# Optimization experiments

Hardware: AMD Instinct MI355X
Metric: run time of the kernel (lower is better)

Reference implementation:

```python
import jax, jax.numpy as jnp
import numpy as np

INF = 10000.0

# ---------- differentiable (jax) pieces ----------

def _embed(x, W1, b1, W2, b2):
    # nn.Sequential(Linear, Dropout(eval=identity), ReLU, Linear, ReLU)
    h = jax.nn.relu(x @ W1.T + b1)
    return jax.nn.relu(h @ W2.T + b2)


def _cdist(a, b):
    # batched euclidean cdist with zero-safe sqrt (matches torch.cdist values)
    sq = (jnp.sum(a * a, -1)[:, :, None]
          + jnp.sum(b * b, -1)[:, None, :]
          - 2.0 * jnp.einsum('bnd,bmd->bnm', a, b))
    sq = jnp.maximum(sq, 0.0)
    safe = jnp.where(sq > 0, sq, 1.0)
    return jnp.where(sq > 0, jnp.sqrt(safe), 0.0)


def _edit_costs(x_s, x_t, W1, b1, W2, b2, virtual, B, N):
    D = W2.shape[0]
    es = _embed(x_s, W1, b1, W2, b2).reshape(B, N, D)
    et = _embed(x_t, W1, b1, W2, b2).reshape(B, N, D)
    v = _embed(virtual[None, :], W1, b1, W2, b2)          # [1, D]
    vb = jnp.broadcast_to(v[None, :, :], (B, 1, D))
    es = jnp.concatenate([es, vb], axis=1)                # [B, N+1, D]
    et = jnp.concatenate([et, vb], axis=1)
    d = _cdist(es, et)                                    # [B, N+1, N+1]
    # per-pair normalization: d / sum(d) * (len_s * len_t)
    d = d / jnp.sum(d, axis=(1, 2), keepdims=True) * float(N * N)
    return d

# ---------- host-side LSAPE (replaces scipy.optimize.linear_sum_assignment) ----------

def _lsap(C):
    # Jonker-Volgenant / shortest augmenting path, square cost matrix.
    n = C.shape[0]
    u = np.zeros(n + 1)
    v = np.zeros(n + 1)
    p = np.zeros(n + 1, np.int64)    # p[j] = row matched to column j (1-indexed)
    way = np.zeros(n + 1, np.int64)
    for i in range(1, n + 1):
        p[0] = i
        j0 = 0
        minv = np.full(n + 1, np.inf)
        used = np.zeros(n + 1, bool)
        while True:
            used[j0] = True
            i0 = p[j0]
            free = np.nonzero(~used)[0]
            cur = C[i0 - 1, free - 1] - u[i0] - v[free]
            better = cur < minv[free]
            minv[free] = np.where(better, cur, minv[free])
            way[free] = np.where(better, j0, way[free])
            k = int(np.argmin(minv[free]))
            j1 = int(free[k])
            delta = minv[free][k]
            u[p[used]] += delta
            v[used] -= delta
            minv[free] -= delta
            j0 = j1
            if p[j0] == 0:
                break
        while j0 != 0:
            j1 = int(way[j0])
            p[j0] = p[j1]
            j0 = j1
    rows = p[1:] - 1
    cols = np.arange(n)
    return rows, cols


def _lsape(ec, n, m):
    # ec: (n+1, m+1) edit costs with virtual row/col; build (n+m)x(n+m) LSAPE matrix
    C = np.zeros((n + m, n + m))
    C[:n, :m] = ec[:n, :m]
    C[n:, :m] = INF
    C[:n, m:] = INF
    C[np.arange(n, n + m), np.arange(m)] = ec[n, :m]       # insertions
    C[np.arange(n), np.arange(m, m + n)] = ec[:n, m]       # deletions
    C[~np.isfinite(C)] = INF
    q, p = _lsap(C)
    A = np.zeros((n + 1, m + 1), np.int64)
    A[np.minimum(q, n), np.minimum(p, m)] = 1
    A[-1, -1] = 0
    return A

# ---------- harness ----------

def setup_inputs() -> dict:
    B, N, FIN, D = 16, 128, 512, 512
    key = jax.random.key(0)
    ks = jax.random.split(key, 7)
    s1 = 1.0 / np.sqrt(FIN)
    s2 = 1.0 / np.sqrt(D)
    return {
        'x_s': jax.random.normal(ks[0], (B * N, FIN), jnp.float32),
        'x_t': jax.random.normal(ks[1], (B * N, FIN), jnp.float32),
        'W1': jax.random.uniform(ks[2], (D, FIN), jnp.float32, -s1, s1),
        'b1': jax.random.uniform(ks[3], (D,), jnp.float32, -s1, s1),
        'W2': jax.random.uniform(ks[4], (D, D), jnp.float32, -s2, s2),
        'b2': jax.random.uniform(ks[5], (D,), jnp.float32, -s2, s2),
        'virtual': jax.random.uniform(ks[6], (FIN,), jnp.float32),
        'npairs': 16,
        'n_nodes': 128,
    }


def reference(x_s, x_t, W1, b1, W2, b2, virtual, npairs, n_nodes):
    B, N = int(npairs), int(n_nodes)
    edit = _edit_costs(x_s, x_t, W1, b1, W2, b2, virtual, B, N)  # [B, N+1, N+1]
    ec_np = np.asarray(jax.device_get(edit), np.float64)
    aligns = np.stack([_lsape(ec_np[i], N, N) for i in range(B)])
    A = jnp.asarray(aligns)                                      # [B, N+1, N+1] int
    geds = jnp.sum(A * edit, axis=(1, 2)) / float(2 * N)         # / (len_s + len_t)
    return (A, edit, geds)
```

## Files before the change

kernel.cpp:

```cpp
#include <hip/hip_runtime.h>

#define BATCH 16
#define NNODE 128
#define DIM 512
#define NP1 129
#define EDSZ (NP1 * NP1)
#define BIGF 3.0e38f

__global__ __launch_bounds__(256) void gemm2_nt_relu(
    const float* __restrict__ X0, const float* __restrict__ X1,
    const float* __restrict__ W, const float* __restrict__ bias,
    float* __restrict__ Y0, float* __restrict__ Y1,
    int M, int N, int K) {
  const float* X = blockIdx.z ? X1 : X0;
  float* Y = blockIdx.z ? Y1 : Y0;
  __shared__ float sA[32][68];
  __shared__ float sB[32][68];
  const int tid = threadIdx.x;
  const int m0 = blockIdx.x * 64;
  const int n0 = blockIdx.y * 64;
  const int tm = tid / 16, tn = tid % 16;
  const int lr = tid >> 2;
  const int lk8 = (tid & 3) * 8;
  float acc[4][4] = {};
  for (int k0 = 0; k0 < K; k0 += 32) {
    const float* xa = X + (size_t)(m0 + lr) * K + k0 + lk8;
    const float* wb = W + (size_t)(n0 + lr) * K + k0 + lk8;
    float4 a0 = *(const float4*)(xa);
    float4 a1 = *(const float4*)(xa + 4);
    float4 b0 = *(const float4*)(wb);
    float4 b1 = *(const float4*)(wb + 4);
    sA[lk8 + 0][lr] = a0.x; sA[lk8 + 1][lr] = a0.y;
    sA[lk8 + 2][lr] = a0.z; sA[lk8 + 3][lr] = a0.w;
    sA[lk8 + 4][lr] = a1.x; sA[lk8 + 5][lr] = a1.y;
    sA[lk8 + 6][lr] = a1.z; sA[lk8 + 7][lr] = a1.w;
    sB[lk8 + 0][lr] = b0.x; sB[lk8 + 1][lr] = b0.y;
    sB[lk8 + 2][lr] = b0.z; sB[lk8 + 3][lr] = b0.w;
    sB[lk8 + 4][lr] = b1.x; sB[lk8 + 5][lr] = b1.y;
    sB[lk8 + 6][lr] = b1.z; sB[lk8 + 7][lr] = b1.w;
    __syncthreads();
#pragma unroll
    for (int k = 0; k < 32; ++k) {
      const float4 a = *(const float4*)&sA[k][tm * 4];
      const float4 b = *(const float4*)&sB[k][tn * 4];
      acc[0][0] = fmaf(a.x, b.x, acc[0][0]);
      acc[0][1] = fmaf(a.x, b.y, acc[0][1]);
      acc[0][2] = fmaf(a.x, b.z, acc[0][2]);
      acc[0][3] = fmaf(a.x, b.w, acc[0][3]);
      acc[1][0] = fmaf(a.y, b.x, acc[1][0]);
      acc[1][1] = fmaf(a.y, b.y, acc[1][1]);
      acc[1][2] = fmaf(a.y, b.z, acc[1][2]);
      acc[1][3] = fmaf(a.y, b.w, acc[1][3]);
      acc[2][0] = fmaf(a.z, b.x, acc[2][0]);
      acc[2][1] = fmaf(a.z, b.y, acc[2][1]);
      acc[2][2] = fmaf(a.z, b.z, acc[2][2]);
      acc[2][3] = fmaf(a.z, b.w, acc[2][3]);
      acc[3][0] = fmaf(a.w, b.x, acc[3][0]);
      acc[3][1] = fmaf(a.w, b.y, acc[3][1]);
      acc[3][2] = fmaf(a.w, b.z, acc[3][2]);
      acc[3][3] = fmaf(a.w, b.w, acc[3][3]);
    }
    __syncthreads();
  }
#pragma unroll
  for (int i = 0; i < 4; ++i) {
    int m = m0 + tm * 4 + i;
#pragma unroll
    for (int j = 0; j < 4; ++j) {
      int n = n0 + tn * 4 + j;
      Y[(size_t)m * N + n] = fmaxf(acc[i][j] + bias[n], 0.f);
    }
  }
}

__global__ __launch_bounds__(256) void virt_embed(
    const float* __restrict__ x,
    const float* __restrict__ W1, const float* __restrict__ b1,
    const float* __restrict__ W2, const float* __restrict__ b2,
    float* __restrict__ e_v) {
  __shared__ float sx[DIM];
  __shared__ float sh[DIM];
  for (int k = threadIdx.x; k < DIM; k += 256) sx[k] = x[k];
  __syncthreads();
  for (int n = threadIdx.x; n < DIM; n += 256) {
    const float* w = W1 + (size_t)n * DIM;
    float s = 0.f;
    for (int k = 0; k < DIM; k += 4) {
      float4 wv = *(const float4*)(w + k);
      s = fmaf(sx[k + 0], wv.x, s);
      s = fmaf(sx[k + 1], wv.y, s);
      s = fmaf(sx[k + 2], wv.z, s);
      s = fmaf(sx[k + 3], wv.w, s);
    }
    sh[n] = fmaxf(s + b1[n], 0.f);
  }
  __syncthreads();
  for (int n = threadIdx.x; n < DIM; n += 256) {
    const float* w = W2 + (size_t)n * DIM;
    float s = 0.f;
    for (int k = 0; k < DIM; k += 4) {
      float4 wv = *(const float4*)(w + k);
      s = fmaf(sh[k + 0], wv.x, s);
      s = fmaf(sh[k + 1], wv.y, s);
      s = fmaf(sh[k + 2], wv.z, s);
      s = fmaf(sh[k + 3], wv.w, s);
    }
    e_v[n] = fmaxf(s + b2[n], 0.f);
  }
}

__global__ __launch_bounds__(256) void cdist_kernel(
    const float* __restrict__ es, const float* __restrict__ et,
    const float* __restrict__ ev, float* __restrict__ d) {
  const int b = blockIdx.z;
  const int i0 = blockIdx.x * 32;
  const int j0 = blockIdx.y * 32;
  __shared__ float sA[32][33];
  __shared__ float sB[32][33];
  const int tid = threadIdx.x;
  const int ty = tid / 16, tx = tid % 16;
  const int lr = tid / 8;
  const int lk4 = (tid % 8) * 4;
  const int gi = i0 + lr;
  const int gj = j0 + lr;
  const float* pa = (gi < NNODE) ? (es + ((size_t)b * NNODE + gi) * DIM) : ev;
  const float* pb = (gj < NNODE) ? (et + ((size_t)b * NNODE + gj) * DIM) : ev;
  float acc[2][2] = {};
  for (int k0 = 0; k0 < DIM; k0 += 32) {
    float4 av = *(const float4*)(pa + k0 + lk4);
    float4 bv = *(const float4*)(pb + k0 + lk4);
    sA[lr][lk4 + 0] = av.x; sA[lr][lk4 + 1] = av.y;
    sA[lr][lk4 + 2] = av.z; sA[lr][lk4 + 3] = av.w;
    sB[lr][lk4 + 0] = bv.x; sB[lr][lk4 + 1] = bv.y;
    sB[lr][lk4 + 2] = bv.z; sB[lr][lk4 + 3] = bv.w;
    __syncthreads();
#pragma unroll 8
    for (int k = 0; k < 32; ++k) {
      float a0 = sA[ty * 2 + 0][k], a1 = sA[ty * 2 + 1][k];
      float b0 = sB[tx * 2 + 0][k], b1 = sB[tx * 2 + 1][k];
      float d00 = a0 - b0, d01 = a0 - b1, d10 = a1 - b0, d11 = a1 - b1;
      acc[0][0] = fmaf(d00, d00, acc[0][0]);
      acc[0][1] = fmaf(d01, d01, acc[0][1]);
      acc[1][0] = fmaf(d10, d10, acc[1][0]);
      acc[1][1] = fmaf(d11, d11, acc[1][1]);
    }
    __syncthreads();
  }
#pragma unroll
  for (int i = 0; i < 2; ++i) {
    int gi2 = i0 + ty * 2 + i;
#pragma unroll
    for (int j = 0; j < 2; ++j) {
      int gj2 = j0 + tx * 2 + j;
      if (gi2 < NP1 && gj2 < NP1)
        d[(size_t)b * EDSZ + gi2 * NP1 + gj2] = sqrtf(acc[i][j]);
    }
  }
}

__global__ __launch_bounds__(256) void batch_sum(
    const float* __restrict__ d, float* __restrict__ sums) {
  const int b = blockIdx.x;
  double s = 0.0;
  for (int idx = threadIdx.x; idx < EDSZ; idx += 256)
    s += (double)d[(size_t)b * EDSZ + idx];
  __shared__ double red[256];
  red[threadIdx.x] = s;
  __syncthreads();
  for (int off = 128; off; off >>= 1) {
    if (threadIdx.x < off) red[threadIdx.x] += red[threadIdx.x + off];
    __syncthreads();
  }
  if (threadIdx.x == 0) sums[b] = (float)red[0];
}

__global__ __launch_bounds__(256) void normalize_kernel(
    const float* __restrict__ d, const float* __restrict__ sums,
    float* __restrict__ edit) {
  int idx = blockIdx.x * 256 + threadIdx.x;
  if (idx < BATCH * EDSZ) {
    int b = idx / EDSZ;
    edit[idx] = d[idx] / sums[b] * (float)(NNODE * NNODE);
  }
}

__device__ __forceinline__ unsigned key_of(float m, int col) {
  return (__float_as_uint(m) & 0xFFFFFF80u) | (unsigned)col;
}

template <int CTRL>
__device__ __forceinline__ unsigned dpp_umin_step(unsigned x) {
  const unsigned o = (unsigned)__builtin_amdgcn_update_dpp(
      (int)0xFFFFFFFFu, (int)x, CTRL, 0xf, 0xf, false);
  return o < x ? o : x;
}

__device__ __forceinline__ unsigned wave_umin_key(unsigned x) {
  x = dpp_umin_step<0x111>(x);
  x = dpp_umin_step<0x112>(x);
  x = dpp_umin_step<0x114>(x);
  x = dpp_umin_step<0x118>(x);
  x = dpp_umin_step<0x142>(x);
  x = dpp_umin_step<0x143>(x);
  return (unsigned)__builtin_amdgcn_readlane((int)x, 63);
}

template <int CTRL>
__device__ __forceinline__ void dpp_umin2_step(unsigned& m1, unsigned& m2) {
  const unsigned o1 = (unsigned)__builtin_amdgcn_update_dpp(
      (int)0xFFFFFFFFu, (int)m1, CTRL, 0xf, 0xf, false);
  const unsigned o2 = (unsigned)__builtin_amdgcn_update_dpp(
      (int)0xFFFFFFFFu, (int)m2, CTRL, 0xf, 0xf, false);
  const unsigned lo = m1 < o1 ? m1 : o1;
  const unsigned hi = m1 < o1 ? o1 : m1;
  const unsigned yo = m2 < o2 ? m2 : o2;
  m1 = lo;
  m2 = hi < yo ? hi : yo;
}

__device__ __forceinline__ void wave_umin2_key(unsigned a, unsigned b,
                                               unsigned& k1, unsigned& k2) {
  unsigned m1 = a < b ? a : b;
  unsigned m2 = a < b ? b : a;
  dpp_umin2_step<0x111>(m1, m2);
  dpp_umin2_step<0x112>(m1, m2);
  dpp_umin2_step<0x114>(m1, m2);
  dpp_umin2_step<0x118>(m1, m2);
  dpp_umin2_step<0x142>(m1, m2);
  dpp_umin2_step<0x143>(m1, m2);
  k1 = (unsigned)__builtin_amdgcn_readlane((int)m1, 63);
  k2 = (unsigned)__builtin_amdgcn_readlane((int)m2, 63);
}

__device__ __forceinline__ float fsel2(float a0, float a1, int s) {
  return (s == 0) ? a0 : a1;
}
__device__ __forceinline__ int isel2(int a0, int a1, int s) {
  return (s == 0) ? a0 : a1;
}
__device__ __forceinline__ float readlane_f32(float x, int lane) {
  return __uint_as_float(
      (unsigned)__builtin_amdgcn_readlane((int)__float_as_uint(x), lane));
}

__global__ __launch_bounds__(64) void lsap_kernel(
    const float* __restrict__ edit, float* __restrict__ Aout,
    float* __restrict__ geds) {
  const int b = blockIdx.x;
  const float* ec = edit + (size_t)b * EDSZ;
  float* A = Aout + (size_t)b * EDSZ;
  const int lane = threadIdx.x;
  const int cbase = lane * 2;

  __shared__ float D[NNODE * NNODE];

  for (int idx = lane; idx < NNODE * NNODE; idx += 64) {
    const int i = idx >> 7, j = idx & 127;
    const float sub = ec[i * NP1 + j];
    const float di = ec[i * NP1 + NNODE] + ec[NNODE * NP1 + j];
    D[idx] = fminf(sub, di);
  }
  for (int idx = lane; idx < EDSZ; idx += 64) A[idx] = 0.f;
  __syncthreads();

  float u0 = 0.f, u1 = 0.f;
  float v0 = 0.f, v1 = 0.f;
  float m0, m1;
  int w0 = 0, w1 = 0;
  int p0 = 0, p1 = 0;
  int x0 = 0, x1 = 0;

  int y0 = 0, y1 = 0;
  {
    float c0 = BIGF, c1 = BIGF;
    for (int r = 0; r < NNODE; ++r) {
      const float2 f = *(const float2*)&D[r * NNODE + cbase];
      if (f.x < c0) { c0 = f.x; y0 = r; }
      if (f.y < c1) { c1 = f.y; y1 = r; }
    }
    v0 = c0; v1 = c1;
  }

  unsigned long long ra0 = 0, ra1 = 0;
  for (int j = 0; j < NNODE; ++j) {
    const int jl = j >> 1, jq = j & 1;
    const int i1 = __builtin_amdgcn_readlane(isel2(y0, y1, jq), jl);
    const int bit = i1 & 63;
    const unsigned long long msk = (i1 < 64) ? ra0 : ra1;
    if (!((msk >> bit) & 1ull)) {
      if (i1 < 64) ra0 |= 1ull << bit; else ra1 |= 1ull << bit;
      if (lane == jl) {
        if (jq == 0) p0 = i1 + 1;
        else p1 = i1 + 1;
      }
      if (lane == (i1 >> 1)) {
        if ((i1 & 1) == 0) x0 = j + 1;
        else x1 = j + 1;
      }
    }
  }

  for (int ii = 0; ii < NNODE; ++ii) {
    const int xj = __builtin_amdgcn_readlane(isel2(x0, x1, ii & 1), ii >> 1);
    if (xj == 0) continue;
    const int j1 = xj - 1;
    const float2 f = *(const float2*)&D[ii * NNODE + cbase];
    float r0 = fmaxf(f.x - v0, 0.f);
    float r1 = fmaxf(f.y - v1, 0.f);
    if (cbase + 0 == j1) r0 = BIGF;
    if (cbase + 1 == j1) r1 = BIGF;
    const unsigned ka = key_of(r0, cbase + 0);
    const unsigned kb = key_of(r1, cbase + 1);
    const unsigned kmin = wave_umin_key(ka < kb ? ka : kb);
    const int jm = (int)(kmin & 127u);
    const float umin = readlane_f32(fsel2(r0, r1, jm & 1), jm >> 1);
    if (lane == (j1 >> 1)) {
      if ((j1 & 1) == 0) v0 -= umin; else v1 -= umin;
    }
    if (lane == (ii >> 1)) {
      if ((ii & 1) == 0) u0 = umin; else u1 = umin;
    }
  }

  {
    const int nfree0 =
        NNODE - __builtin_popcountll(ra0) - __builtin_popcountll(ra1);
    const int budget = 2 * nfree0 + 8;
    for (int step = 0; step < budget; ++step) {
      const unsigned long long fm0 = ~ra0, fm1 = ~ra1;
      int i;
      if (fm0) i = __builtin_ctzll(fm0);
      else if (fm1) i = 64 + __builtin_ctzll(fm1);
      else break;

      const float2 f = *(const float2*)&D[i * NNODE + cbase];
      const float r0 = fmaxf(f.x - v0, 0.f);
      const float r1 = fmaxf(f.y - v1, 0.f);
      unsigned k1, k2;
      wave_umin2_key(key_of(r0, cbase + 0), key_of(r1, cbase + 1), k1, k2);
      const int j1 = (int)(k1 & 127u), j2 = (int)(k2 & 127u);
      const float u1v = readlane_f32(fsel2(r0, r1, j1 & 1), j1 >> 1);
      const float u2v = readlane_f32(fsel2(r0, r1, j2 & 1), j2 >> 1);

      int jt = j1;
      int i1 = __builtin_amdgcn_readlane(isel2(p0, p1, j1 & 1), j1 >> 1);
      if (u1v < u2v) {
        const float dv = u2v - u1v;
        if (lane == (j1 >> 1)) {
          if ((j1 & 1) == 0) v0 -= dv; else v1 -= dv;
        }
      } else if (i1 != 0) {
        jt = j2;
        i1 = __builtin_amdgcn_readlane(isel2(p0, p1, j2 & 1), j2 >> 1);
      }
      if (lane == (jt >> 1)) {
        if ((jt & 1) == 0) p0 = i + 1; else p1 = i + 1;
      }
      if (lane == (i >> 1)) {
        if ((i & 1) == 0) u0 = u2v; else u1 = u2v;
      }
      if (i < 64) ra0 |= 1ull << i; else ra1 |= 1ull << (i - 64);
      if (i1 != 0) {
        const int rr = i1 - 1;
        if (rr < 64) ra0 &= ~(1ull << rr); else ra1 &= ~(1ull << (rr - 64));
        if (lane == (rr >> 1)) {
          if ((rr & 1) == 0) u0 = 0.f; else u1 = 0.f;
        }
      }
    }
  }

  for (int ii = 0; ii < NNODE; ++ii) {
    const unsigned long long amsk = (ii < 64) ? ra0 : ra1;
    if ((amsk >> (ii & 63)) & 1ull) continue;
    const int i = ii + 1;

    unsigned cused = 0, rused = 0;
    m0 = m1 = BIGF;
    int j0 = 0;
    int i0 = i;
    for (int guard = 0; guard <= NNODE; ++guard) {
      if (j0 > 0 && lane == ((j0 - 1) >> 1)) {
        if (((j0 - 1) & 1) == 0) { cused |= 1u; m0 = BIGF; }
        else { cused |= 2u; m1 = BIGF; }
      }
      if (lane == ((i0 - 1) >> 1)) rused |= 1u << ((i0 - 1) & 1);

      const float u_i0 = readlane_f32(fsel2(u0, u1, (i0 - 1) & 1), (i0 - 1) >> 1);

      const float2 f = *(const float2*)&D[(i0 - 1) * NNODE + cbase];

      const bool f0 = !(cused & 1u), f1 = !(cused & 2u);
      {
        float cur = fmaxf(f.x - u_i0 - v0, 0.f);
        bool up = f0 && (cur < m0);
        m0 = up ? cur : m0; w0 = up ? j0 : w0;
      }
      {
        float cur = fmaxf(f.y - u_i0 - v1, 0.f);
        bool up = f1 && (cur < m1);
        m1 = up ? cur : m1; w1 = up ? j0 : w1;
      }

      const unsigned ka = key_of(m0, cbase + 0);
      const unsigned kb = key_of(m1, cbase + 1);
      const unsigned kmin = wave_umin_key(ka < kb ? ka : kb);
      const int jcol = (int)(kmin & 127u);
      const float delta = readlane_f32(fsel2(m0, m1, jcol & 1), jcol >> 1);
      const int j1 = jcol + 1;

      if (!f0) v0 -= delta; else m0 = fmaxf(m0 - delta, 0.f);
      if (!f1) v1 -= delta; else m1 = fmaxf(m1 - delta, 0.f);
      if (rused & 1u) u0 += delta;
      if (rused & 2u) u1 += delta;

      const int pj1 = __builtin_amdgcn_readlane(
          isel2(p0, p1, (j1 - 1) & 1), (j1 - 1) >> 1);
      j0 = j1;
      if (pj1 == 0) break;
      i0 = pj1;
    }

    int jc = j0;
    while (jc != 0) {
      const int cl = (jc - 1) >> 1, cq = (jc - 1) & 1;
      const int jp = __builtin_amdgcn_readlane(isel2(w0, w1, cq), cl);
      const int js = (jp == 0) ? 1 : jp;
      const int pvr = __builtin_amdgcn_readlane(
          isel2(p0, p1, (js - 1) & 1), (js - 1) >> 1);
      const int pv = (jp == 0) ? i : pvr;
      if (lane == cl) {
        if (cq == 0) p0 = pv;
        else p1 = pv;
      }
      jc = jp;
    }
  }

  double contrib = 0.0;
  {
    const int pr[2] = {p0, p1};
#pragma unroll
    for (int q = 0; q < 2; ++q) {
      const int j = cbase + q;
      const int i = pr[q] - 1;
      const float sub = ec[i * NP1 + j];
      const float di = ec[i * NP1 + NNODE] + ec[NNODE * NP1 + j];
      if (sub < di) {
        A[i * NP1 + j] = 1.f;
        contrib += (double)sub;
      } else {
        A[i * NP1 + NNODE] = 1.f;
        A[NNODE * NP1 + j] = 1.f;
        contrib += (double)di;
      }
    }
  }
#pragma unroll
  for (int off = 32; off; off >>= 1) contrib += __shfl_xor(contrib, off);
  if (lane == 0) geds[b] = (float)(contrib / 256.0);
}

extern "C" void kernel_launch(void* const* d_in, const int* in_sizes, int n_in,
                              void* d_out, int out_size, void* d_ws, size_t ws_size,
                              hipStream_t stream) {
  const float* x_s  = (const float*)d_in[0];
  const float* x_t  = (const float*)d_in[1];
  const float* W1   = (const float*)d_in[2];
  const float* b1   = (const float*)d_in[3];
  const float* W2   = (const float*)d_in[4];
  const float* b2   = (const float*)d_in[5];
  const float* virt = (const float*)d_in[6];

  const int M = BATCH * NNODE;

  float* ws    = (float*)d_ws;
  float* h_s   = ws;
  float* h_t   = h_s + (size_t)M * DIM;
  float* e_s   = h_t + (size_t)M * DIM;
  float* e_t   = e_s + (size_t)M * DIM;
  float* e_v   = e_t + (size_t)M * DIM;
  float* d_raw = e_v + DIM;
  float* sums  = d_raw + (size_t)BATCH * EDSZ;

  float* Aout = (float*)d_out;
  float* edit = Aout + (size_t)BATCH * EDSZ;
  float* geds = edit + (size_t)BATCH * EDSZ;

  dim3 gblk(M / 64, DIM / 64, 2);
  virt_embed<<<1, 256, 0, stream>>>(virt, W1, b1, W2, b2, e_v);
  gemm2_nt_relu<<<gblk, 256, 0, stream>>>(x_s, x_t, W1, b1, h_s, h_t, M, DIM, DIM);
  gemm2_nt_relu<<<gblk, 256, 0, stream>>>(h_s, h_t, W2, b2, e_s, e_t, M, DIM, DIM);

  cdist_kernel<<<dim3(5, 5, BATCH), 256, 0, stream>>>(e_s, e_t, e_v, d_raw);
  batch_sum<<<BATCH, 256, 0, stream>>>(d_raw, sums);
  normalize_kernel<<<(BATCH * EDSZ + 255) / 256, 256, 0, stream>>>(d_raw, sums, edit);
  lsap_kernel<<<BATCH, 64, 0, stream>>>(edit, Aout, geds);
}
```

Before: 823.6 us.

## Interleave two LSAP problems per wavefront and precompute reduced cost matrix

```diff
diff --git a/kernel.cpp b/kernel.cpp
--- a/kernel.cpp
+++ b/kernel.cpp
@@ -184,6 +184,18 @@
   }
 }
 
+__global__ __launch_bounds__(256) void build_D(
+    const float* __restrict__ edit, float* __restrict__ Dg) {
+  int idx = blockIdx.x * 256 + threadIdx.x;
+  if (idx < BATCH * NNODE * NNODE) {
+    const int b = idx >> 14;
+    const int rc = idx & 16383;
+    const int i = rc >> 7, j = rc & 127;
+    const float* ec = edit + (size_t)b * EDSZ;
+    Dg[idx] = fminf(ec[i * NP1 + j], ec[i * NP1 + NNODE] + ec[NNODE * NP1 + j]);
+  }
+}
+
 __device__ __forceinline__ unsigned key_of(float m, int col) {
   return (__float_as_uint(m) & 0xFFFFFF80u) | (unsigned)col;
 }
@@ -243,203 +255,267 @@
       (unsigned)__builtin_amdgcn_readlane((int)__float_as_uint(x), lane));
 }
 
-__global__ __launch_bounds__(64) void lsap_kernel(
-    const float* __restrict__ edit, float* __restrict__ Aout,
-    float* __restrict__ geds) {
-  const int b = blockIdx.x;
-  const float* ec = edit + (size_t)b * EDSZ;
-  float* A = Aout + (size_t)b * EDSZ;
+__global__ __launch_bounds__(64) void lsap2_kernel(
+    const float* __restrict__ edit, const float* __restrict__ Dg,
+    float* __restrict__ Aout, float* __restrict__ geds) {
+  const int bid = blockIdx.x;
   const int lane = threadIdx.x;
   const int cbase = lane * 2;
-
-  __shared__ float D[NNODE * NNODE];
-
-  for (int idx = lane; idx < NNODE * NNODE; idx += 64) {
-    const int i = idx >> 7, j = idx & 127;
-    const float sub = ec[i * NP1 + j];
-    const float di = ec[i * NP1 + NNODE] + ec[NNODE * NP1 + j];
-    D[idx] = fminf(sub, di);
-  }
-  for (int idx = lane; idx < EDSZ; idx += 64) A[idx] = 0.f;
+  const float* DgA = Dg + (size_t)(2 * bid + 0) * (NNODE * NNODE);
+  const float* DgB = Dg + (size_t)(2 * bid + 1) * (NNODE * NNODE);
+
+  __shared__ float DL[NNODE * NNODE];
+
+  for (int idx = lane * 4; idx < NNODE * NNODE; idx += 256)
+    *(float4*)&DL[idx] = *(const float4*)&DgA[idx];
+  {
+    float* A0 = Aout + (size_t)(2 * bid + 0) * EDSZ;
+    float* A1 = Aout + (size_t)(2 * bid + 1) * EDSZ;
+    for (int idx = lane; idx < EDSZ; idx += 64) { A0[idx] = 0.f; A1[idx] = 0.f; }
+  }
   __syncthreads();
 
-  float u0 = 0.f, u1 = 0.f;
-  float v0 = 0.f, v1 = 0.f;
-  float m0, m1;
-  int w0 = 0, w1 = 0;
-  int p0 = 0, p1 = 0;
-  int x0 = 0, x1 = 0;
-
-  int y0 = 0, y1 = 0;
+  float u0c[2] = {0.f, 0.f}, u1c[2] = {0.f, 0.f};
+  float v0c[2], v1c[2], m0c[2], m1c[2];
+  int w0c[2] = {0, 0}, w1c[2] = {0, 0};
+  int p0c[2] = {0, 0}, p1c[2] = {0, 0};
+  int x0c[2] = {0, 0}, x1c[2] = {0, 0};
+  unsigned long long ra0c[2] = {0ull, 0ull}, ra1c[2] = {0ull, 0ull};
+
+  int y0c[2], y1c[2];
   {
-    float c0 = BIGF, c1 = BIGF;
+    float c0[2] = {BIGF, BIGF}, c1[2] = {BIGF, BIGF};
+    int yy0[2] = {0, 0}, yy1[2] = {0, 0};
     for (int r = 0; r < NNODE; ++r) {
-      const float2 f = *(const float2*)&D[r * NNODE + cbase];
-      if (f.x < c0) { c0 = f.x; y0 = r; }
-      if (f.y < c1) { c1 = f.y; y1 = r; }
-    }
-    v0 = c0; v1 = c1;
-  }
-
-  unsigned long long ra0 = 0, ra1 = 0;
-  for (int j = 0; j < NNODE; ++j) {
-    const int jl = j >> 1, jq = j & 1;
-    const int i1 = __builtin_amdgcn_readlane(isel2(y0, y1, jq), jl);
-    const int bit = i1 & 63;
-    const unsigned long long msk = (i1 < 64) ? ra0 : ra1;
-    if (!((msk >> bit) & 1ull)) {
-      if (i1 < 64) ra0 |= 1ull << bit; else ra1 |= 1ull << bit;
-      if (lane == jl) {
-        if (jq == 0) p0 = i1 + 1;
-        else p1 = i1 + 1;
-      }
-      if (lane == (i1 >> 1)) {
-        if ((i1 & 1) == 0) x0 = j + 1;
-        else x1 = j + 1;
+      const float2 fa = *(const float2*)&DL[r * NNODE + cbase];
+      const float2 fb = *(const float2*)&DgB[r * NNODE + cbase];
+      if (fa.x < c0[0]) { c0[0] = fa.x; yy0[0] = r; }
+      if (fa.y < c1[0]) { c1[0] = fa.y; yy1[0] = r; }
+      if (fb.x < c0[1]) { c0[1] = fb.x; yy0[1] = r; }
+      if (fb.y < c1[1]) { c1[1] = fb.y; yy1[1] = r; }
+    }
+#pragma unroll
+    for (int c = 0; c < 2; ++c) {
+      v0c[c] = c0[c]; v1c[c] = c1[c]; y0c[c] = yy0[c]; y1c[c] = yy1[c];
+    }
+  }
+
+#pragma unroll
+  for (int c = 0; c < 2; ++c) {
+    for (int j = 0; j < NNODE; ++j) {
+      const int jl = j >> 1, jq = j & 1;
+      const int i1 = __builtin_amdgcn_readlane(isel2(y0c[c], y1c[c], jq), jl);
+      const int bit = i1 & 63;
+      const unsigned long long msk = (i1 < 64) ? ra0c[c] : ra1c[c];
+      if (!((msk >> bit) & 1ull)) {
+        if (i1 < 64) ra0c[c] |= 1ull << bit; else ra1c[c] |= 1ull << bit;
+        if (lane == jl) {
+          if (jq == 0) p0c[c] = i1 + 1; else p1c[c] = i1 + 1;
+        }
+        if (lane == (i1 >> 1)) {
+          if ((i1 & 1) == 0) x0c[c] = j + 1; else x1c[c] = j + 1;
+        }
       }
     }
   }
 
   for (int ii = 0; ii < NNODE; ++ii) {
-    const int xj = __builtin_amdgcn_readlane(isel2(x0, x1, ii & 1), ii >> 1);
-    if (xj == 0) continue;
-    const int j1 = xj - 1;
-    const float2 f = *(const float2*)&D[ii * NNODE + cbase];
-    float r0 = fmaxf(f.x - v0, 0.f);
-    float r1 = fmaxf(f.y - v1, 0.f);
-    if (cbase + 0 == j1) r0 = BIGF;
-    if (cbase + 1 == j1) r1 = BIGF;
-    const unsigned ka = key_of(r0, cbase + 0);
-    const unsigned kb = key_of(r1, cbase + 1);
-    const unsigned kmin = wave_umin_key(ka < kb ? ka : kb);
-    const int jm = (int)(kmin & 127u);
-    const float umin = readlane_f32(fsel2(r0, r1, jm & 1), jm >> 1);
-    if (lane == (j1 >> 1)) {
-      if ((j1 & 1) == 0) v0 -= umin; else v1 -= umin;
-    }
-    if (lane == (ii >> 1)) {
-      if ((ii & 1) == 0) u0 = umin; else u1 = umin;
+    const float2 fa = *(const float2*)&DL[ii * NNODE + cbase];
+    const float2 fb = *(const float2*)&DgB[ii * NNODE + cbase];
+    const float2 f[2] = {fa, fb};
+#pragma unroll
+    for (int c = 0; c < 2; ++c) {
+      const int xj =
+          __builtin_amdgcn_readlane(isel2(x0c[c], x1c[c], ii & 1), ii >> 1);
+      const int j1 = xj - 1;
+      float r0 = fmaxf(f[c].x - v0c[c], 0.f);
+      float r1 = fmaxf(f[c].y - v1c[c], 0.f);
+      if (cbase + 0 == j1) r0 = BIGF;
+      if (cbase + 1 == j1) r1 = BIGF;
+      const unsigned ka = key_of(r0, cbase + 0);
+      const unsigned kb = key_of(r1, cbase + 1);
+      const unsigned kmin = wave_umin_key(ka < kb ? ka : kb);
+      const int jm = (int)(kmin & 127u);
+      const float umin = readlane_f32(fsel2(r0, r1, jm & 1), jm >> 1);
+      if (xj != 0) {
+        if (lane == (j1 >> 1)) {
+          if ((j1 & 1) == 0) v0c[c] -= umin; else v1c[c] -= umin;
+        }
+        if (lane == (ii >> 1)) {
+          if ((ii & 1) == 0) u0c[c] = umin; else u1c[c] = umin;
+        }
+      }
     }
   }
 
   {
-    const int nfree0 =
-        NNODE - __builtin_popcountll(ra0) - __builtin_popcountll(ra1);
-    const int budget = 2 * nfree0 + 8;
-    for (int step = 0; step < budget; ++step) {
-      const unsigned long long fm0 = ~ra0, fm1 = ~ra1;
-      int i;
-      if (fm0) i = __builtin_ctzll(fm0);
-      else if (fm1) i = 64 + __builtin_ctzll(fm1);
-      else break;
-
-      const float2 f = *(const float2*)&D[i * NNODE + cbase];
-      const float r0 = fmaxf(f.x - v0, 0.f);
-      const float r1 = fmaxf(f.y - v1, 0.f);
-      unsigned k1, k2;
-      wave_umin2_key(key_of(r0, cbase + 0), key_of(r1, cbase + 1), k1, k2);
-      const int j1 = (int)(k1 & 127u), j2 = (int)(k2 & 127u);
-      const float u1v = readlane_f32(fsel2(r0, r1, j1 & 1), j1 >> 1);
-      const float u2v = readlane_f32(fsel2(r0, r1, j2 & 1), j2 >> 1);
-
-      int jt = j1;
-      int i1 = __builtin_amdgcn_readlane(isel2(p0, p1, j1 & 1), j1 >> 1);
-      if (u1v < u2v) {
-        const float dv = u2v - u1v;
-        if (lane == (j1 >> 1)) {
-          if ((j1 & 1) == 0) v0 -= dv; else v1 -= dv;
-        }
-      } else if (i1 != 0) {
-        jt = j2;
-        i1 = __builtin_amdgcn_readlane(isel2(p0, p1, j2 & 1), j2 >> 1);
-      }
-      if (lane == (jt >> 1)) {
-        if ((jt & 1) == 0) p0 = i + 1; else p1 = i + 1;
-      }
-      if (lane == (i >> 1)) {
-        if ((i & 1) == 0) u0 = u2v; else u1 = u2v;
-      }
-      if (i < 64) ra0 |= 1ull << i; else ra1 |= 1ull << (i - 64);
-      if (i1 != 0) {
-        const int rr = i1 - 1;
-        if (rr < 64) ra0 &= ~(1ull << rr); else ra1 &= ~(1ull << (rr - 64));
-        if (lane == (rr >> 1)) {
-          if ((rr & 1) == 0) u0 = 0.f; else u1 = 0.f;
-        }
-      }
-    }
-  }
-
-  for (int ii = 0; ii < NNODE; ++ii) {
-    const unsigned long long amsk = (ii < 64) ? ra0 : ra1;
-    if ((amsk >> (ii & 63)) & 1ull) continue;
-    const int i = ii + 1;
-
-    unsigned cused = 0, rused = 0;
-    m0 = m1 = BIGF;
-    int j0 = 0;
-    int i0 = i;
-    for (int guard = 0; guard <= NNODE; ++guard) {
-      if (j0 > 0 && lane == ((j0 - 1) >> 1)) {
-        if (((j0 - 1) & 1) == 0) { cused |= 1u; m0 = BIGF; }
-        else { cused |= 2u; m1 = BIGF; }
-      }
-      if (lane == ((i0 - 1) >> 1)) rused |= 1u << ((i0 - 1) & 1);
-
-      const float u_i0 = readlane_f32(fsel2(u0, u1, (i0 - 1) & 1), (i0 - 1) >> 1);
-
-      const float2 f = *(const float2*)&D[(i0 - 1) * NNODE + cbase];
-
-      const bool f0 = !(cused & 1u), f1 = !(cused & 2u);
-      {
-        float cur = fmaxf(f.x - u_i0 - v0, 0.f);
-        bool up = f0 && (cur < m0);
-        m0 = up ? cur : m0; w0 = up ? j0 : w0;
-      }
-      {
-        float cur = fmaxf(f.y - u_i0 - v1, 0.f);
-        bool up = f1 && (cur < m1);
-        m1 = up ? cur : m1; w1 = up ? j0 : w1;
-      }
-
-      const unsigned ka = key_of(m0, cbase + 0);
-      const unsigned kb = key_of(m1, cbase + 1);
-      const unsigned kmin = wave_umin_key(ka < kb ? ka : kb);
-      const int jcol = (int)(kmin & 127u);
-      const float delta = readlane_f32(fsel2(m0, m1, jcol & 1), jcol >> 1);
-      const int j1 = jcol + 1;
-
-      if (!f0) v0 -= delta; else m0 = fmaxf(m0 - delta, 0.f);
-      if (!f1) v1 -= delta; else m1 = fmaxf(m1 - delta, 0.f);
-      if (rused & 1u) u0 += delta;
-      if (rused & 2u) u1 += delta;
-
-      const int pj1 = __builtin_amdgcn_readlane(
-          isel2(p0, p1, (j1 - 1) & 1), (j1 - 1) >> 1);
-      j0 = j1;
-      if (pj1 == 0) break;
-      i0 = pj1;
-    }
-
-    int jc = j0;
-    while (jc != 0) {
-      const int cl = (jc - 1) >> 1, cq = (jc - 1) & 1;
-      const int jp = __builtin_amdgcn_readlane(isel2(w0, w1, cq), cl);
-      const int js = (jp == 0) ? 1 : jp;
-      const int pvr = __builtin_amdgcn_readlane(
-          isel2(p0, p1, (js - 1) & 1), (js - 1) >> 1);
-      const int pv = (jp == 0) ? i : pvr;
-      if (lane == cl) {
-        if (cq == 0) p0 = pv;
-        else p1 = pv;
-      }
-      jc = jp;
-    }
-  }
-
-  double contrib = 0.0;
-  {
-    const int pr[2] = {p0, p1};
+    int budget[2];
+#pragma unroll
+    for (int c = 0; c < 2; ++c) {
+      const int nf = NNODE - __builtin_popcountll(ra0c[c]) -
+                     __builtin_popcountll(ra1c[c]);
+      budget[c] = 2 * nf + 8;
+    }
+    for (;;) {
+      int iRow[2];
+      bool act[2];
+#pragma unroll
+      for (int c = 0; c < 2; ++c) {
+        const unsigned long long fm0 = ~ra0c[c], fm1 = ~ra1c[c];
+        act[c] = (budget[c] > 0) && ((fm0 | fm1) != 0ull);
+        iRow[c] = fm0 ? __builtin_ctzll(fm0)
+                      : (fm1 ? 64 + __builtin_ctzll(fm1) : 0);
+        if (act[c]) budget[c]--;
+      }
+      if (!act[0] && !act[1]) break;
+      const float2 fa = *(const float2*)&DL[iRow[0] * NNODE + cbase];
+      const float2 fb = *(const float2*)&DgB[iRow[1] * NNODE + cbase];
+      const float2 f[2] = {fa, fb};
+#pragma unroll
+      for (int c = 0; c < 2; ++c) {
+        const int i = iRow[c];
+        const float r0 = fmaxf(f[c].x - v0c[c], 0.f);
+        const float r1 = fmaxf(f[c].y - v1c[c], 0.f);
+        unsigned k1, k2;
+        wave_umin2_key(key_of(r0, cbase + 0), key_of(r1, cbase + 1), k1, k2);
+        const int j1 = (int)(k1 & 127u), j2 = (int)(k2 & 127u);
+        const float u1v = readlane_f32(fsel2(r0, r1, j1 & 1), j1 >> 1);
+        const float u2v = readlane_f32(fsel2(r0, r1, j2 & 1), j2 >> 1);
+        int jt = j1;
+        int i1 = __builtin_amdgcn_readlane(isel2(p0c[c], p1c[c], j1 & 1), j1 >> 1);
+        const bool lowered = (u1v < u2v);
+        if (!lowered && i1 != 0) {
+          jt = j2;
+          i1 = __builtin_amdgcn_readlane(isel2(p0c[c], p1c[c], j2 & 1), j2 >> 1);
+        }
+        if (act[c]) {
+          if (lowered) {
+            const float dv = u2v - u1v;
+            if (lane == (j1 >> 1)) {
+              if ((j1 & 1) == 0) v0c[c] -= dv; else v1c[c] -= dv;
+            }
+          }
+          if (lane == (jt >> 1)) {
+            if ((jt & 1) == 0) p0c[c] = i + 1; else p1c[c] = i + 1;
+          }
+          if (lane == (i >> 1)) {
+            if ((i & 1) == 0) u0c[c] = u2v; else u1c[c] = u2v;
+          }
+          if (i < 64) ra0c[c] |= 1ull << i; else ra1c[c] |= 1ull << (i - 64);
+          if (i1 != 0) {
+            const int rr = i1 - 1;
+            if (rr < 64) ra0c[c] &= ~(1ull << rr);
+            else ra1c[c] &= ~(1ull << (rr - 64));
+            if (lane == (rr >> 1)) {
+              if ((rr & 1) == 0) u0c[c] = 0.f; else u1c[c] = 0.f;
+            }
+          }
+        }
+      }
+    }
+  }
+
+  for (;;) {
+    int iP[2];
+    bool act[2];
+#pragma unroll
+    for (int c = 0; c < 2; ++c) {
+      const unsigned long long fm0 = ~ra0c[c], fm1 = ~ra1c[c];
+      act[c] = ((fm0 | fm1) != 0ull);
+      iP[c] = fm0 ? (__builtin_ctzll(fm0) + 1)
+                  : (fm1 ? (64 + __builtin_ctzll(fm1) + 1) : 1);
+    }
+    if (!act[0] && !act[1]) break;
+
+    unsigned cused[2] = {0u, 0u}, rused[2] = {0u, 0u};
+    int j0[2] = {0, 0}, i0[2];
+    bool pact[2];
+#pragma unroll
+    for (int c = 0; c < 2; ++c) {
+      m0c[c] = BIGF; m1c[c] = BIGF;
+      i0[c] = iP[c];
+      pact[c] = act[c];
+    }
+    for (int guard = 0; guard <= 2 * NNODE && (pact[0] || pact[1]); ++guard) {
+      const float2 fa = *(const float2*)&DL[(i0[0] - 1) * NNODE + cbase];
+      const float2 fb = *(const float2*)&DgB[(i0[1] - 1) * NNODE + cbase];
+      const float2 f[2] = {fa, fb};
+#pragma unroll
+      for (int c = 0; c < 2; ++c) {
+        {
+          const bool mk = pact[c] && j0[c] > 0 && lane == ((j0[c] - 1) >> 1);
+          if (mk) {
+            if (((j0[c] - 1) & 1) == 0) { cused[c] |= 1u; m0c[c] = BIGF; }
+            else { cused[c] |= 2u; m1c[c] = BIGF; }
+          }
+          if (pact[c] && lane == ((i0[c] - 1) >> 1))
+            rused[c] |= 1u << ((i0[c] - 1) & 1);
+        }
+        const float u_i0 =
+            readlane_f32(fsel2(u0c[c], u1c[c], (i0[c] - 1) & 1), (i0[c] - 1) >> 1);
+        const bool f0 = !(cused[c] & 1u), f1 = !(cused[c] & 2u);
+        {
+          float cur = fmaxf(f[c].x - u_i0 - v0c[c], 0.f);
+          bool up = pact[c] && f0 && (cur < m0c[c]);
+          m0c[c] = up ? cur : m0c[c];
+          w0c[c] = up ? j0[c] : w0c[c];
+        }
+        {
+          float cur = fmaxf(f[c].y - u_i0 - v1c[c], 0.f);
+          bool up = pact[c] && f1 && (cur < m1c[c]);
+          m1c[c] = up ? cur : m1c[c];
+          w1c[c] = up ? j0[c] : w1c[c];
+        }
+        const unsigned ka = key_of(m0c[c], cbase + 0);
+        const unsigned kb = key_of(m1c[c], cbase + 1);
+        const unsigned kmin = wave_umin_key(ka < kb ? ka : kb);
+        const int jcol = (int)(kmin & 127u);
+        const float delta = readlane_f32(fsel2(m0c[c], m1c[c], jcol & 1), jcol >> 1);
+        const int j1 = jcol + 1;
+        if (pact[c]) {
+          if (!f0) v0c[c] -= delta; else m0c[c] = fmaxf(m0c[c] - delta, 0.f);
+          if (!f1) v1c[c] -= delta; else m1c[c] = fmaxf(m1c[c] - delta, 0.f);
+          if (rused[c] & 1u) u0c[c] += delta;
+          if (rused[c] & 2u) u1c[c] += delta;
+        }
+        const int pj1 = __builtin_amdgcn_readlane(
+            isel2(p0c[c], p1c[c], (j1 - 1) & 1), (j1 - 1) >> 1);
+        if (pact[c]) {
+          j0[c] = j1;
+          if (pj1 == 0) pact[c] = false;
+          else i0[c] = pj1;
+        }
+      }
+    }
+#pragma unroll
+    for (int c = 0; c < 2; ++c) {
+      if (act[c]) {
+        int jc = j0[c];
+        while (jc != 0) {
+          const int cl = (jc - 1) >> 1, cq = (jc - 1) & 1;
+          const int jp = __builtin_amdgcn_readlane(isel2(w0c[c], w1c[c], cq), cl);
+          const int js = (jp == 0) ? 1 : jp;
+          const int pvr = __builtin_amdgcn_readlane(
+              isel2(p0c[c], p1c[c], (js - 1) & 1), (js - 1) >> 1);
+          const int pv = (jp == 0) ? iP[c] : pvr;
+          if (lane == cl) {
+            if (cq == 0) p0c[c] = pv; else p1c[c] = pv;
+          }
+          jc = jp;
+        }
+        const int r = iP[c] - 1;
+        if (r < 64) ra0c[c] |= 1ull << r; else ra1c[c] |= 1ull << (r - 64);
+      }
+    }
+  }
+
+#pragma unroll
+  for (int c = 0; c < 2; ++c) {
+    const int b = 2 * bid + c;
+    const float* ec = edit + (size_t)b * EDSZ;
+    float* A = Aout + (size_t)b * EDSZ;
+    double contrib = 0.0;
+    const int pr[2] = {p0c[c], p1c[c]};
 #pragma unroll
     for (int q = 0; q < 2; ++q) {
       const int j = cbase + q;
@@ -455,10 +531,10 @@
         contrib += (double)di;
       }
     }
-  }
-#pragma unroll
-  for (int off = 32; off; off >>= 1) contrib += __shfl_xor(contrib, off);
-  if (lane == 0) geds[b] = (float)(contrib / 256.0);
+#pragma unroll
+    for (int off = 32; off; off >>= 1) contrib += __shfl_xor(contrib, off);
+    if (lane == 0) geds[b] = (float)(contrib / 256.0);
+  }
 }
 
 extern "C" void kernel_launch(void* const* d_in, const int* in_sizes, int n_in,
@@ -482,6 +558,7 @@
   float* e_v   = e_t + (size_t)M * DIM;
   float* d_raw = e_v + DIM;
   float* sums  = d_raw + (size_t)BATCH * EDSZ;
+  float* Dg    = sums + 16;
 
   float* Aout = (float*)d_out;
   float* edit = Aout + (size_t)BATCH * EDSZ;
@@ -495,5 +572,6 @@
   cdist_kernel<<<dim3(5, 5, BATCH), 256, 0, stream>>>(e_s, e_t, e_v, d_raw);
   batch_sum<<<BATCH, 256, 0, stream>>>(d_raw, sums);
   normalize_kernel<<<(BATCH * EDSZ + 255) / 256, 256, 0, stream>>>(d_raw, sums, edit);
-  lsap_kernel<<<BATCH, 64, 0, stream>>>(edit, Aout, geds);
-}
+  build_D<<<(BATCH * NNODE * NNODE + 255) / 256, 256, 0, stream>>>(edit, Dg);
+  lsap2_kernel<<<BATCH / 2, 64, 0, stream>>>(edit, Dg, Aout, geds);
+}
```

Result: slower. 1.663 ms (+101.9%).
